# Kernel tuning notes

Measured on AMD Instinct MI355X. Metric: run time of the kernel, lower is better.

The kernel has to match this reference:

```python
import jax, jax.numpy as jnp
import numpy as np

B, T, C = 32, 1024, 1024
N_LAYER, LAYER_ID, FIRST_SA = 12, 3, 1
RWKV_K_CLAMP = 60.0
RWKV_K_EPS = 1e-16


def _init_params():
    # decay_speed init exactly as in RWKV_TimeMix.__init__
    f1 = 3.0 + (LAYER_ID - FIRST_SA) / (N_LAYER - 1 - FIRST_SA) * (1.2 - 3.0)
    f2 = 0.65 + (LAYER_ID - FIRST_SA) / (N_LAYER - 1 - FIRST_SA) * (0.4 - 0.65)
    h = np.arange(C, dtype=np.float64)
    decay_speed = np.power(f2, h / (C - 1) * 7) * f1
    time_decay = np.log(decay_speed).astype(np.float32)          # (C,)
    time_first = np.full((C,), np.log(0.3), dtype=np.float32)     # (C,)
    tm = np.ones((C,), dtype=np.float32)
    tm[: C // 2] = 0.0                                            # time_mix
    return jnp.asarray(time_decay), jnp.asarray(time_first), jnp.asarray(tm)


def setup_inputs() -> dict:
    key = jax.random.key(0)
    ks = jax.random.split(key, 5)
    x = jax.random.normal(ks[0], (B, T, C), dtype=jnp.float32)
    scale = 0.02
    Wk = jax.random.normal(ks[1], (C, C), dtype=jnp.float32) * scale
    Wv = jax.random.normal(ks[2], (C, C), dtype=jnp.float32) * scale
    Wr = jax.random.normal(ks[3], (C, C), dtype=jnp.float32) * scale
    Wo = jax.random.normal(ks[4], (C, C), dtype=jnp.float32) * scale
    time_decay, time_first, time_mix = _init_params()
    return {"x": x, "time_decay": time_decay, "time_first": time_first,
            "time_mix": time_mix, "Wk": Wk, "Wv": Wv, "Wr": Wr, "Wo": Wo}


def _wkv(decay, first_w, y, eps):
    # out[b,t,c] = eps + first_w[c]*y[b,t,c] + sum_{u<t} decay[c]^(t-1-u) * y[b,u,c]
    # computed as a linear recurrence S[t] = decay*S[t-1] + y[t] via associative scan.
    a = jnp.broadcast_to(decay, y.shape)
    def comb(l, r):
        a1, b1 = l
        a2, b2 = r
        return (a1 * a2, a2 * b1 + b2)
    _, S = jax.lax.associative_scan(comb, (a, y), axis=1)
    S_prev = jnp.pad(S, ((0, 0), (1, 0), (0, 0)))[:, :-1]  # S[t-1], S[-1]=0
    return eps + first_w * y + S_prev


def reference(x, time_decay, time_first, time_mix, Wk, Wv, Wr, Wo):
    Bn, Tn, Cn = x.shape
    # time shift: ZeroPad2d((0,0,1,-1)) -> shifted[t] = x[t-1], shifted[0]=0
    xs = jnp.pad(x, ((0, 0), (1, 0), (0, 0)))[:, :-1]
    xm = x * time_mix + xs * (1.0 - time_mix)
    k = xm @ Wk.T
    v = xm @ Wv.T
    r = xm @ Wr.T
    k = jnp.exp(jnp.minimum(k, RWKV_K_CLAMP))
    kv = k * v
    decay = jnp.exp(-jnp.exp(time_decay))   # lag-d weight (d>=1): decay^(d-1)
    first_w = jnp.exp(time_first)           # lag-0 weight
    wkv = _wkv(decay, first_w, kv, 0.0)
    wk = _wkv(decay, first_w, k, RWKV_K_EPS)
    rwkv = jax.nn.sigmoid(r) * (wkv / wk)
    return rwkv @ Wo.T
```

## Files before the change

kernel.cpp:

```cpp
#include <hip/hip_runtime.h>


#define DEV __device__ __forceinline__

constexpr int Bc = 32, Tc = 1024, Cc = 1024;
constexpr int Mdim = Bc * Tc;
constexpr int Ndim = Cc;
constexpr int Kdim = Cc;
constexpr int NT = Kdim / 64;
constexpr int CHUNK = 128;
constexpr int LOOKB = 128;
constexpr int NCH = Tc / CHUNK;

typedef short bf16x8 __attribute__((ext_vector_type(8)));
typedef float f32x4  __attribute__((ext_vector_type(4)));

DEV unsigned short f2bf(float f) {
    unsigned u = __float_as_uint(f);
    u += 0x7FFFu + ((u >> 16) & 1u);
    return (unsigned short)(u >> 16);
}
DEV float bf2f(unsigned short s) { return __uint_as_float(((unsigned)s) << 16); }

DEV void gload16(const unsigned short* g, const unsigned short* l) {
    __builtin_amdgcn_global_load_lds(
        (const __attribute__((address_space(1))) void*)g,
        (__attribute__((address_space(3))) void*)l, 16, 0, 0);
}

__global__ void wconv_kernel(const float* __restrict__ w0, const float* __restrict__ w1,
                             const float* __restrict__ w2, const float* __restrict__ w3,
                             unsigned short* __restrict__ d0, unsigned short* __restrict__ d1,
                             unsigned short* __restrict__ d2, unsigned short* __restrict__ d3) {
    int i = blockIdx.x * blockDim.x + threadIdx.x;
    const float* src = (blockIdx.y == 0) ? w0 : (blockIdx.y == 1) ? w1 : (blockIdx.y == 2) ? w2 : w3;
    unsigned short* dst = (blockIdx.y == 0) ? d0 : (blockIdx.y == 1) ? d1 : (blockIdx.y == 2) ? d2 : d3;
    float4 v = ((const float4*)src)[i];
    ((ushort4*)dst)[i] = make_ushort4(f2bf(v.x), f2bf(v.y), f2bf(v.z), f2bf(v.w));
}

__global__ void xm_kernel(const float* __restrict__ x, const float* __restrict__ tm,
                          unsigned short* __restrict__ xm) {
    int i4 = blockIdx.x * blockDim.x + threadIdx.x;
    int c4 = i4 & (Cc / 4 - 1);
    int t  = (i4 >> 8) & (Tc - 1);
    float4 xc = ((const float4*)x)[i4];
    float4 xp = make_float4(0.f, 0.f, 0.f, 0.f);
    if (t > 0) xp = ((const float4*)x)[i4 - Cc / 4];
    float4 tv = ((const float4*)tm)[c4];
    ushort4 o = make_ushort4(
        f2bf(xc.x * tv.x + xp.x * (1.f - tv.x)),
        f2bf(xc.y * tv.y + xp.y * (1.f - tv.y)),
        f2bf(xc.z * tv.z + xp.z * (1.f - tv.z)),
        f2bf(xc.w * tv.w + xp.w * (1.f - tv.w)));
    ((ushort4*)xm)[i4] = o;
}

template <int MODE>
__global__ __launch_bounds__(512, 2) void gemm256_kernel(
    const unsigned short* __restrict__ A,
    const unsigned short* __restrict__ W,
    void* __restrict__ out)
{
    __shared__ unsigned short lds[2 * 32768];

    const int tid = threadIdx.x;
    const int l = tid & 63, w = tid >> 6;
    const int wr = w >> 2, wc = w & 3;
    const int l15 = l & 15, l4 = l >> 4;
    const size_t row0 = (size_t)blockIdx.y * 256;
    const int col0 = blockIdx.x * 256;

    const int rs = tid >> 3;
    const int cs = ((tid & 7) ^ ((tid >> 3) & 7)) << 3;
    const int swz = (l15 & 7) << 3;

    f32x4 acc[8][4];
#pragma unroll
    for (int m = 0; m < 8; m++)
#pragma unroll
        for (int n = 0; n < 4; n++)
#pragma unroll
            for (int q = 0; q < 4; q++) acc[m][n][q] = 0.f;

#define STAGE(kt, bb) {                                                                \
    _Pragma("unroll")                                                                  \
    for (int g = 0; g < 4; g++)                                                        \
        gload16(A + (row0 + g * 64 + rs) * (size_t)Kdim + (kt) + cs,                   \
                lds + (bb) * 32768 + g * 4096 + w * 512);                              \
    _Pragma("unroll")                                                                  \
    for (int g = 0; g < 4; g++)                                                        \
        gload16(W + (size_t)(col0 + g * 64 + rs) * Kdim + (kt) + cs,                   \
                lds + (bb) * 32768 + 16384 + g * 4096 + w * 512); }

    STAGE(0, 0)
    asm volatile("s_waitcnt vmcnt(0)" ::: "memory");
    __builtin_amdgcn_s_barrier();

    for (int t = 0; t < NT; t++) {
        const int b = t & 1;
        const unsigned short* Ab = lds + b * 32768;
        const unsigned short* Bb = Ab + 16384;
        bf16x8 af0[4][2], af1[4][2], bf0[2][2], bf1[2][2];

#pragma unroll
        for (int mi = 0; mi < 4; mi++)
#pragma unroll
            for (int kk = 0; kk < 2; kk++)
                af0[mi][kk] = *(const bf16x8*)(Ab + (wr * 128 + mi * 16 + l15) * 64 + ((kk * 32 + l4 * 8) ^ swz));
#pragma unroll
        for (int n = 0; n < 2; n++)
#pragma unroll
            for (int kk = 0; kk < 2; kk++)
                bf0[n][kk] = *(const bf16x8*)(Bb + (wc * 64 + n * 16 + l15) * 64 + ((kk * 32 + l4 * 8) ^ swz));
        if (t < NT - 1) STAGE((t + 1) * 64, b ^ 1)
        __builtin_amdgcn_s_barrier();
        asm volatile("s_waitcnt lgkmcnt(0)" ::: "memory");
        __builtin_amdgcn_s_setprio(1);
#pragma unroll
        for (int mi = 0; mi < 4; mi++)
#pragma unroll
            for (int n = 0; n < 2; n++)
#pragma unroll
                for (int kk = 0; kk < 2; kk++)
                    acc[mi][n] = __builtin_amdgcn_mfma_f32_16x16x32_bf16(af0[mi][kk], bf0[n][kk], acc[mi][n], 0, 0, 0);
        __builtin_amdgcn_s_setprio(0);

#pragma unroll
        for (int n = 0; n < 2; n++)
#pragma unroll
            for (int kk = 0; kk < 2; kk++)
                bf1[n][kk] = *(const bf16x8*)(Bb + (wc * 64 + (2 + n) * 16 + l15) * 64 + ((kk * 32 + l4 * 8) ^ swz));
        __builtin_amdgcn_s_barrier();
        asm volatile("s_waitcnt lgkmcnt(0)" ::: "memory");
        __builtin_amdgcn_s_setprio(1);
#pragma unroll
        for (int mi = 0; mi < 4; mi++)
#pragma unroll
            for (int n = 0; n < 2; n++)
#pragma unroll
                for (int kk = 0; kk < 2; kk++)
                    acc[mi][2 + n] = __builtin_amdgcn_mfma_f32_16x16x32_bf16(af0[mi][kk], bf1[n][kk], acc[mi][2 + n], 0, 0, 0);
        __builtin_amdgcn_s_setprio(0);

#pragma unroll
        for (int mi = 0; mi < 4; mi++)
#pragma unroll
            for (int kk = 0; kk < 2; kk++)
                af1[mi][kk] = *(const bf16x8*)(Ab + (wr * 128 + (4 + mi) * 16 + l15) * 64 + ((kk * 32 + l4 * 8) ^ swz));
        __builtin_amdgcn_s_barrier();
        asm volatile("s_waitcnt lgkmcnt(0)" ::: "memory");
        __builtin_amdgcn_s_setprio(1);
#pragma unroll
        for (int mi = 0; mi < 4; mi++)
#pragma unroll
            for (int n = 0; n < 2; n++)
#pragma unroll
                for (int kk = 0; kk < 2; kk++)
                    acc[4 + mi][n] = __builtin_amdgcn_mfma_f32_16x16x32_bf16(af1[mi][kk], bf0[n][kk], acc[4 + mi][n], 0, 0, 0);
        __builtin_amdgcn_s_setprio(0);

        if (t < NT - 1) { asm volatile("s_waitcnt vmcnt(0)" ::: "memory"); }
        __builtin_amdgcn_s_barrier();
        __builtin_amdgcn_s_setprio(1);
#pragma unroll
        for (int mi = 0; mi < 4; mi++)
#pragma unroll
            for (int n = 0; n < 2; n++)
#pragma unroll
                for (int kk = 0; kk < 2; kk++)
                    acc[4 + mi][2 + n] = __builtin_amdgcn_mfma_f32_16x16x32_bf16(af1[mi][kk], bf1[n][kk], acc[4 + mi][2 + n], 0, 0, 0);
        __builtin_amdgcn_s_setprio(0);
    }
#undef STAGE

#pragma unroll
    for (int m = 0; m < 8; m++)
#pragma unroll
        for (int n = 0; n < 4; n++)
#pragma unroll
            for (int q = 0; q < 4; q++) {
                size_t row = row0 + wr * 128 + m * 16 + l4 * 4 + q;
                int col = col0 + wc * 64 + n * 16 + l15;
                size_t idx = row * Ndim + col;
                float v = acc[m][n][q];
                if constexpr (MODE == 0)
                    ((unsigned short*)out)[idx] = f2bf(__expf(fminf(v, 60.f)));
                else if constexpr (MODE == 1)
                    ((unsigned short*)out)[idx] = f2bf(v);
                else if constexpr (MODE == 2)
                    ((unsigned short*)out)[idx] = f2bf(1.f / (1.f + __expf(-v)));
                else
                    ((float*)out)[idx] = v;
            }
}

__global__ __launch_bounds__(64) void scan_kernel(
    const unsigned short* __restrict__ kexp, const unsigned short* __restrict__ vb,
    const unsigned short* __restrict__ sr,
    const float* __restrict__ td, const float* __restrict__ tf,
    unsigned short* __restrict__ rwkv)
{
    int c = (blockIdx.x * blockDim.x + threadIdx.x) * 2;
    int ch = blockIdx.y;
    int b  = blockIdx.z;
    int t0 = ch * CHUNK;
    int tstart = t0 - LOOKB; if (tstart < 0) tstart = 0;

    float d0 = __expf(-__expf(td[c]));
    float d1 = __expf(-__expf(td[c + 1]));
    float f0 = __expf(tf[c]);
    float f1 = __expf(tf[c + 1]);
    float Skv0 = 0.f, Sk0 = 0.f, Skv1 = 0.f, Sk1 = 0.f;

    size_t base = (size_t)b * Tc * Cc + c;
    size_t idx = base + (size_t)tstart * Cc;
#pragma unroll 4
    for (int t = tstart; t < t0; t++, idx += Cc) {
        ushort2 ke = *(const ushort2*)(kexp + idx);
        ushort2 vv = *(const ushort2*)(vb + idx);
        float k0 = bf2f(ke.x), k1 = bf2f(ke.y);
        float y0 = k0 * bf2f(vv.x), y1 = k1 * bf2f(vv.y);
        Skv0 = d0 * Skv0 + y0; Sk0 = d0 * Sk0 + k0;
        Skv1 = d1 * Skv1 + y1; Sk1 = d1 * Sk1 + k1;
    }
#pragma unroll 4
    for (int t = t0; t < t0 + CHUNK; t++, idx += Cc) {
        ushort2 ke = *(const ushort2*)(kexp + idx);
        ushort2 vv = *(const ushort2*)(vb + idx);
        ushort2 sg = *(const ushort2*)(sr + idx);
        float k0 = bf2f(ke.x), k1 = bf2f(ke.y);
        float y0 = k0 * bf2f(vv.x), y1 = k1 * bf2f(vv.y);
        float wkv0 = f0 * y0 + Skv0, wkv1 = f1 * y1 + Skv1;
        float wk0 = 1e-16f + f0 * k0 + Sk0, wk1 = 1e-16f + f1 * k1 + Sk1;
        ushort2 o;
        o.x = f2bf(bf2f(sg.x) * (wkv0 / wk0));
        o.y = f2bf(bf2f(sg.y) * (wkv1 / wk1));
        *(ushort2*)(rwkv + idx) = o;
        Skv0 = d0 * Skv0 + y0; Sk0 = d0 * Sk0 + k0;
        Skv1 = d1 * Skv1 + y1; Sk1 = d1 * Sk1 + k1;
    }
}

extern "C" void kernel_launch(void* const* d_in, const int* in_sizes, int n_in,
                              void* d_out, int out_size, void* d_ws, size_t ws_size,
                              hipStream_t stream) {
    const float* x  = (const float*)d_in[0];
    const float* td = (const float*)d_in[1];
    const float* tf = (const float*)d_in[2];
    const float* tm = (const float*)d_in[3];
    const float* Wk = (const float*)d_in[4];
    const float* Wv = (const float*)d_in[5];
    const float* Wr = (const float*)d_in[6];
    const float* Wo = (const float*)d_in[7];

    const size_t BTC = (size_t)Bc * Tc * Cc;
    const size_t WN  = (size_t)Cc * Cc;

    char* ws = (char*)d_ws;
    unsigned short* wkb   = (unsigned short*)ws; ws += WN * 2;
    unsigned short* wvb   = (unsigned short*)ws; ws += WN * 2;
    unsigned short* wrb   = (unsigned short*)ws; ws += WN * 2;
    unsigned short* wob   = (unsigned short*)ws; ws += WN * 2;
    unsigned short* xm    = (unsigned short*)ws; ws += BTC * 2;
    unsigned short* kexpb = (unsigned short*)ws; ws += BTC * 2;
    unsigned short* vbb   = (unsigned short*)ws; ws += BTC * 2;
    unsigned short* srb   = (unsigned short*)ws; ws += BTC * 2;
    float* outp = (float*)d_out;

    wconv_kernel<<<dim3(WN / 1024, 4), 256, 0, stream>>>(Wk, Wv, Wr, Wo, wkb, wvb, wrb, wob);

    xm_kernel<<<BTC / 4 / 256, 256, 0, stream>>>(x, tm, xm);

    dim3 ggrid(Ndim / 256, Mdim / 256);
    gemm256_kernel<0><<<ggrid, 512, 0, stream>>>(xm, wkb, (void*)kexpb);
    gemm256_kernel<1><<<ggrid, 512, 0, stream>>>(xm, wvb, (void*)vbb);
    gemm256_kernel<2><<<ggrid, 512, 0, stream>>>(xm, wrb, (void*)srb);

    scan_kernel<<<dim3(Cc / 128, NCH, Bc), 64, 0, stream>>>(kexpb, vbb, srb, td, tf, xm);

    gemm256_kernel<3><<<ggrid, 512, 0, stream>>>(xm, wob, (void*)outp);
}
```

Before: 446.3 us.

## Restructure GEMM main loop per k-slice and swap grid block ordering

The GEMM inner loop moves from four quadrant phases, each separated by a barrier, to two k-slice phases. Each phase loads all 8 A and 4 B fragments and issues 32 MFMAs, and the next tile's A and B global-to-LDS copies are split across the two phases. The intra-iteration barriers go away, leaving one barrier per k-tile. The grid is also transposed so consecutive blocks walk along M with the same weight column tile, which changes L2 reuse of A and W. Register pressure rises with 12 live fragments per phase, and removing barriers loosens wave synchronisation, which may affect LDS timing.

```diff
diff --git a/kernel.cpp b/kernel.cpp
--- a/kernel.cpp
+++ b/kernel.cpp
@@ -68,8 +68,8 @@
     const int l = tid & 63, w = tid >> 6;
     const int wr = w >> 2, wc = w & 3;
     const int l15 = l & 15, l4 = l >> 4;
-    const size_t row0 = (size_t)blockIdx.y * 256;
-    const int col0 = blockIdx.x * 256;
+    const size_t row0 = (size_t)blockIdx.x * 256;
+    const int col0 = blockIdx.y * 256;
 
     const int rs = tid >> 3;
     const int cs = ((tid & 7) ^ ((tid >> 3) & 7)) << 3;
@@ -83,17 +83,18 @@
 #pragma unroll
             for (int q = 0; q < 4; q++) acc[m][n][q] = 0.f;
 
-#define STAGE(kt, bb) {                                                                \
+#define STAGE_A(kt, bb) {                                                              \
     _Pragma("unroll")                                                                  \
     for (int g = 0; g < 4; g++)                                                        \
         gload16(A + (row0 + g * 64 + rs) * (size_t)Kdim + (kt) + cs,                   \
-                lds + (bb) * 32768 + g * 4096 + w * 512);                              \
+                lds + (bb) * 32768 + g * 4096 + w * 512); }
+#define STAGE_B(kt, bb) {                                                              \
     _Pragma("unroll")                                                                  \
     for (int g = 0; g < 4; g++)                                                        \
         gload16(W + (size_t)(col0 + g * 64 + rs) * Kdim + (kt) + cs,                   \
                 lds + (bb) * 32768 + 16384 + g * 4096 + w * 512); }
 
-    STAGE(0, 0)
+    STAGE_A(0, 0) STAGE_B(0, 0)
     asm volatile("s_waitcnt vmcnt(0)" ::: "memory");
     __builtin_amdgcn_s_barrier();
 
@@ -101,78 +102,34 @@
         const int b = t & 1;
         const unsigned short* Ab = lds + b * 32768;
         const unsigned short* Bb = Ab + 16384;
-        bf16x8 af0[4][2], af1[4][2], bf0[2][2], bf1[2][2];
-
-#pragma unroll
-        for (int mi = 0; mi < 4; mi++)
-#pragma unroll
-            for (int kk = 0; kk < 2; kk++)
-                af0[mi][kk] = *(const bf16x8*)(Ab + (wr * 128 + mi * 16 + l15) * 64 + ((kk * 32 + l4 * 8) ^ swz));
-#pragma unroll
-        for (int n = 0; n < 2; n++)
-#pragma unroll
-            for (int kk = 0; kk < 2; kk++)
-                bf0[n][kk] = *(const bf16x8*)(Bb + (wc * 64 + n * 16 + l15) * 64 + ((kk * 32 + l4 * 8) ^ swz));
-        if (t < NT - 1) STAGE((t + 1) * 64, b ^ 1)
-        __builtin_amdgcn_s_barrier();
-        asm volatile("s_waitcnt lgkmcnt(0)" ::: "memory");
-        __builtin_amdgcn_s_setprio(1);
-#pragma unroll
-        for (int mi = 0; mi < 4; mi++)
-#pragma unroll
-            for (int n = 0; n < 2; n++)
-#pragma unroll
-                for (int kk = 0; kk < 2; kk++)
-                    acc[mi][n] = __builtin_amdgcn_mfma_f32_16x16x32_bf16(af0[mi][kk], bf0[n][kk], acc[mi][n], 0, 0, 0);
-        __builtin_amdgcn_s_setprio(0);
-
-#pragma unroll
-        for (int n = 0; n < 2; n++)
-#pragma unroll
-            for (int kk = 0; kk < 2; kk++)
-                bf1[n][kk] = *(const bf16x8*)(Bb + (wc * 64 + (2 + n) * 16 + l15) * 64 + ((kk * 32 + l4 * 8) ^ swz));
-        __builtin_amdgcn_s_barrier();
-        asm volatile("s_waitcnt lgkmcnt(0)" ::: "memory");
-        __builtin_amdgcn_s_setprio(1);
-#pragma unroll
-        for (int mi = 0; mi < 4; mi++)
-#pragma unroll
-            for (int n = 0; n < 2; n++)
-#pragma unroll
-                for (int kk = 0; kk < 2; kk++)
-                    acc[mi][2 + n] = __builtin_amdgcn_mfma_f32_16x16x32_bf16(af0[mi][kk], bf1[n][kk], acc[mi][2 + n], 0, 0, 0);
-        __builtin_amdgcn_s_setprio(0);
-
-#pragma unroll
-        for (int mi = 0; mi < 4; mi++)
-#pragma unroll
-            for (int kk = 0; kk < 2; kk++)
-                af1[mi][kk] = *(const bf16x8*)(Ab + (wr * 128 + (4 + mi) * 16 + l15) * 64 + ((kk * 32 + l4 * 8) ^ swz));
-        __builtin_amdgcn_s_barrier();
-        asm volatile("s_waitcnt lgkmcnt(0)" ::: "memory");
-        __builtin_amdgcn_s_setprio(1);
-#pragma unroll
-        for (int mi = 0; mi < 4; mi++)
-#pragma unroll
-            for (int n = 0; n < 2; n++)
-#pragma unroll
-                for (int kk = 0; kk < 2; kk++)
-                    acc[4 + mi][n] = __builtin_amdgcn_mfma_f32_16x16x32_bf16(af1[mi][kk], bf0[n][kk], acc[4 + mi][n], 0, 0, 0);
-        __builtin_amdgcn_s_setprio(0);
+
+#pragma unroll
+        for (int kk = 0; kk < 2; kk++) {
+            bf16x8 af[8], bfr[4];
+#pragma unroll
+            for (int mi = 0; mi < 8; mi++)
+                af[mi] = *(const bf16x8*)(Ab + (wr * 128 + mi * 16 + l15) * 64 + ((kk * 32 + l4 * 8) ^ swz));
+#pragma unroll
+            for (int n = 0; n < 4; n++)
+                bfr[n] = *(const bf16x8*)(Bb + (wc * 64 + n * 16 + l15) * 64 + ((kk * 32 + l4 * 8) ^ swz));
+            if (t < NT - 1) {
+                if (kk == 0) STAGE_A((t + 1) * 64, b ^ 1)
+                else         STAGE_B((t + 1) * 64, b ^ 1)
+            }
+            __builtin_amdgcn_s_setprio(1);
+#pragma unroll
+            for (int mi = 0; mi < 8; mi++)
+#pragma unroll
+                for (int n = 0; n < 4; n++)
+                    acc[mi][n] = __builtin_amdgcn_mfma_f32_16x16x32_bf16(af[mi], bfr[n], acc[mi][n], 0, 0, 0);
+            __builtin_amdgcn_s_setprio(0);
+        }
 
         if (t < NT - 1) { asm volatile("s_waitcnt vmcnt(0)" ::: "memory"); }
         __builtin_amdgcn_s_barrier();
-        __builtin_amdgcn_s_setprio(1);
-#pragma unroll
-        for (int mi = 0; mi < 4; mi++)
-#pragma unroll
-            for (int n = 0; n < 2; n++)
-#pragma unroll
-                for (int kk = 0; kk < 2; kk++)
-                    acc[4 + mi][2 + n] = __builtin_amdgcn_mfma_f32_16x16x32_bf16(af1[mi][kk], bf1[n][kk], acc[4 + mi][2 + n], 0, 0, 0);
-        __builtin_amdgcn_s_setprio(0);
     }
-#undef STAGE
+#undef STAGE_A
+#undef STAGE_B
 
 #pragma unroll
     for (int m = 0; m < 8; m++)
@@ -272,7 +229,7 @@
 
     xm_kernel<<<BTC / 4 / 256, 256, 0, stream>>>(x, tm, xm);
 
-    dim3 ggrid(Ndim / 256, Mdim / 256);
+    dim3 ggrid(Mdim / 256, Ndim / 256);
     gemm256_kernel<0><<<ggrid, 512, 0, stream>>>(xm, wkb, (void*)kexpb);
     gemm256_kernel<1><<<ggrid, 512, 0, stream>>>(xm, wvb, (void*)vbb);
     gemm256_kernel<2><<<ggrid, 512, 0, stream>>>(xm, wrb, (void*)srb);
```

Result: no change. 438.4 us (-1.8%).
